# Performance work log

Measured on AMD Instinct MI355X. Metric: run time of the kernel, lower is better.

Reference implementation:

```python
import jax, jax.numpy as jnp
import numpy as np

B, S, E = 2, 2048, 1024
H, D = 16, 64
BASE = 10000.0


def rotate_half(x):
    x1, x2 = jnp.split(x, 2, axis=-1)
    return jnp.concatenate((-x2, x1), axis=-1)


def rope_cos_sin(seq_len, dim):
    inv_freq = 1.0 / (BASE ** (jnp.arange(0, dim, 2, dtype=jnp.float32) / dim))
    t = jnp.arange(seq_len, dtype=jnp.float32)
    freqs = jnp.einsum('i,j->ij', t, inv_freq)          # [S, D/2]
    emb = jnp.concatenate((freqs, freqs), axis=-1)       # [S, D]
    return jnp.cos(emb), jnp.sin(emb)


def setup_inputs() -> dict:
    key = jax.random.key(0)
    ks = jax.random.split(key, 9)
    s = 1.0 / np.sqrt(E)
    inp = {
        'x': jax.random.normal(ks[0], (B, S, E), dtype=jnp.float32),
        'mask': jnp.ones((B, S), dtype=jnp.int32),
        'Wq': jax.random.normal(ks[1], (E, H * D), dtype=jnp.float32) * s,
        'bq': jnp.zeros((H * D,), dtype=jnp.float32),
        'Wk': jax.random.normal(ks[2], (E, H * D), dtype=jnp.float32) * s,
        'bk': jnp.zeros((H * D,), dtype=jnp.float32),
        'Wv': jax.random.normal(ks[3], (E, H * D), dtype=jnp.float32) * s,
        'bv': jnp.zeros((H * D,), dtype=jnp.float32),
        'Wo': jax.random.normal(ks[4], (H * D, E), dtype=jnp.float32) * s,
        'bo': jnp.zeros((E,), dtype=jnp.float32),
    }
    return inp


def reference(x, mask, Wq, bq, Wk, bk, Wv, bv, Wo, bo):
    b, s, _ = x.shape
    scale = D ** (-0.5)
    # projections -> [B, H, S, D]
    q = (x @ Wq + bq).reshape(b, s, H, D).transpose(0, 2, 1, 3)
    k = (x @ Wk + bk).reshape(b, s, H, D).transpose(0, 2, 1, 3)
    v = (x @ Wv + bv).reshape(b, s, H, D).transpose(0, 2, 1, 3)
    # rotary position embedding
    cos, sin = rope_cos_sin(s, D)                      # [S, D]
    cos = cos[None, None]
    sin = sin[None, None]
    q = q * cos + rotate_half(q) * sin
    k = k * cos + rotate_half(k) * sin
    # scores [B, H, S, S]
    scores = jnp.einsum('bhqd,bhkd->bhqk', q, k) * scale
    # padding mask [B,1,1,S]
    scores = jnp.where(mask[:, None, None, :] == 0, -jnp.inf, scores)
    # causal mask
    i = jnp.arange(s)
    causal = jnp.where(i[None, :] > i[:, None], -jnp.inf, 0.0)  # [S, S]
    scores = scores + causal[None, None]
    attn = jax.nn.softmax(scores, axis=-1)
    ctx = jnp.einsum('bhqk,bhkd->bhqd', attn, v)
    ctx = ctx.transpose(0, 2, 1, 3).reshape(b, s, H * D)
    return ctx @ Wo + bo
```

## Files before the change

### kernel.cpp

```cpp
#include <hip/hip_runtime.h>
#include <cstdint>
#include <cstddef>

#define DEVI __device__ __forceinline__

typedef __bf16 bf16_t;
typedef __bf16 bf16x4 __attribute__((ext_vector_type(4)));
typedef __bf16 bf16x8 __attribute__((ext_vector_type(8)));
typedef float  f32x4  __attribute__((ext_vector_type(4)));
typedef float  f32x16 __attribute__((ext_vector_type(16)));
typedef unsigned short u16x4 __attribute__((ext_vector_type(4)));
typedef unsigned int   u32x4 __attribute__((ext_vector_type(4)));

static constexpr int Bz = 2, S = 2048, E = 1024, H = 16, Dh = 64;
static constexpr int M  = Bz * S;
static constexpr int N  = H * Dh;
static constexpr int Kd = E;

DEVI unsigned short f2bf(float f) {
  unsigned u = __builtin_bit_cast(unsigned, f);
  return (unsigned short)((u + 0x7fffu + ((u >> 16) & 1u)) >> 16);
}

DEVI void async_copy16(void* lds, const void* g) {
  __builtin_amdgcn_global_load_lds((__attribute__((address_space(1))) void*)(g),
                                   (__attribute__((address_space(3))) void*)(lds), 16, 0, 0);
}

DEVI void block_sync() { asm volatile("s_barrier" ::: "memory"); }
#define VMCNT4() asm volatile("s_waitcnt vmcnt(4)" ::: "memory")
#define VMCNT0() asm volatile("s_waitcnt vmcnt(0)" ::: "memory")
#define LGKM0()  asm volatile("s_waitcnt lgkmcnt(0)" ::: "memory")

DEVI unsigned cvtpk(float lo, float hi) {
  unsigned r;
  asm("v_cvt_pk_bf16_f32 %0, %1, %2" : "=v"(r) : "v"(lo), "v"(hi));
  return r;
}
DEVI void swap32(unsigned& x, unsigned& y) {
  asm("v_permlane32_swap_b32 %0, %1" : "+v"(x), "+v"(y));
}

__global__ void prep_kernel(const float* __restrict__ x, bf16_t* __restrict__ xb,
                            const float* __restrict__ Wq, const float* __restrict__ Wk,
                            const float* __restrict__ Wv, const float* __restrict__ Wo,
                            bf16_t* __restrict__ WtBase,
                            float* __restrict__ ropeC, float* __restrict__ ropeS) {
  __shared__ unsigned short tile[64][68];
  const int blk = blockIdx.x, tid = threadIdx.x;
  if (blk < 4096) {
    int i = blk * 256 + tid;
    float4 v = ((const float4*)x)[i];
    u16x4 o = { f2bf(v.x), f2bf(v.y), f2bf(v.z), f2bf(v.w) };
    ((u16x4*)xb)[i] = o;
  } else if (blk < 5120) {
    const int i = blk - 4096;
    const int z = i >> 8, rest = i & 255;
    const int n0 = (rest & 15) * 64, k0 = (rest >> 4) * 64;
    const float* W = (z == 0) ? Wq : (z == 1) ? Wk : (z == 2) ? Wv : Wo;
    unsigned short* T = (unsigned short*)(WtBase + (size_t)z * Kd * N);
    for (int e = tid; e < 1024; e += 256) {
      int r = e >> 4, c4 = (e & 15) * 4;
      float4 v = *(const float4*)(W + (size_t)(k0 + r) * N + n0 + c4);
      u16x4 o = { f2bf(v.x), f2bf(v.y), f2bf(v.z), f2bf(v.w) };
      *(u16x4*)&tile[r][c4] = o;
    }
    __syncthreads();
    for (int e = tid; e < 1024; e += 256) {
      int r = e >> 4, c4 = (e & 15) * 4;
      u16x4 o = { tile[c4][r], tile[c4 + 1][r], tile[c4 + 2][r], tile[c4 + 3][r] };
      *(u16x4*)&T[(size_t)(n0 + r) * Kd + k0 + c4] = o;
    }
  } else {
    int i = (blk - 5120) * 256 + tid;
    int pos = i >> 5, j = i & 31;
    float inv = exp2f(-(float)j * 0.41524101186092029f);
    float ang = (float)pos * inv;
    ropeC[i] = cosf(ang);
    ropeS[i] = sinf(ang);
  }
}

__global__ void vtrans_kernel(const bf16_t* __restrict__ V, bf16_t* __restrict__ Vt) {
  __shared__ unsigned short tile[64][68];
  const int bh = blockIdx.y;
  const int s0 = blockIdx.x * 64;
  const unsigned short* Vp = (const unsigned short*)V + (size_t)bh * S * Dh;
  unsigned short* Tp = (unsigned short*)Vt + (size_t)bh * S * Dh;
  const int tid = threadIdx.x;
  for (int e = tid; e < 1024; e += 256) {
    int r = e >> 4, c4 = (e & 15) * 4;
    u16x4 v = *(const u16x4*)(Vp + (size_t)(s0 + r) * Dh + c4);
    *(u16x4*)&tile[r][c4] = v;
  }
  __syncthreads();
  for (int e = tid; e < 1024; e += 256) {
    int d = e >> 4, s4 = (e & 15) * 4;
    int t = (s0 + s4) >> 5, ks = (s0 + s4) & 31;
    u16x4 o = { tile[s4][d], tile[s4 + 1][d], tile[s4 + 2][d], tile[s4 + 3][d] };
    *(u16x4*)&Tp[((size_t)t * Dh + d) * 32 + ks] = o;
  }
}


DEVI void gemm_mainloop(const bf16_t* __restrict__ A, const bf16_t* __restrict__ Bt,
                        bf16_t* sA, bf16_t* sB, int m0, int n0, f32x4 (&acc)[4][4]) {
  const int tid  = threadIdx.x;
  const int lane = tid & 63;
  const int wid  = tid >> 6;
  const int l16  = lane & 15;
  const int quad = lane >> 4;
  const int wm = (wid >> 1) * 64;
  const int wn = (wid & 1) * 64;
  const int o0 = wid * 2048 + lane * 16;
  const int o1 = o0 + 1024;
  const int r0 = o0 >> 6, c0 = o0 & 63;
  const int r1 = o1 >> 6, c1 = o1 & 63;
  const char* Ab = (const char*)A;
  const char* Bb = (const char*)Bt;
  char* sAc = (char*)sA;
  char* sBc = (char*)sB;

  for (int k0 = 0; k0 < Kd; k0 += 32) {
    __syncthreads();
    async_copy16(sAc + wid * 2048,        Ab + ((size_t)(m0 + r0) * Kd + k0) * 2 + c0);
    async_copy16(sAc + wid * 2048 + 1024, Ab + ((size_t)(m0 + r1) * Kd + k0) * 2 + c1);
    async_copy16(sBc + wid * 2048,        Bb + ((size_t)(n0 + r0) * Kd + k0) * 2 + c0);
    async_copy16(sBc + wid * 2048 + 1024, Bb + ((size_t)(n0 + r1) * Kd + k0) * 2 + c1);
    __syncthreads();
    bf16x8 af[4], bfv[4];
#pragma unroll
    for (int mi = 0; mi < 4; ++mi)
      af[mi] = *(const bf16x8*)(sA + (wm + mi * 16 + l16) * 32 + quad * 8);
#pragma unroll
    for (int ni = 0; ni < 4; ++ni)
      bfv[ni] = *(const bf16x8*)(sB + (wn + ni * 16 + l16) * 32 + quad * 8);
#pragma unroll
    for (int mi = 0; mi < 4; ++mi)
#pragma unroll
      for (int ni = 0; ni < 4; ++ni)
        acc[mi][ni] = __builtin_amdgcn_mfma_f32_16x16x32_bf16(af[mi], bfv[ni], acc[mi][ni], 0, 0, 0);
  }
}

__global__ __launch_bounds__(256, 3) void gemm_qkv_kernel(
    const bf16_t* __restrict__ xb, const bf16_t* __restrict__ WtBase,
    const float* __restrict__ bq, const float* __restrict__ bk, const float* __restrict__ bv,
    bf16_t* __restrict__ outBase,
    const float* __restrict__ ropeC, const float* __restrict__ ropeS) {
  __shared__ bf16_t sA[4096], sB[4096];
  const int z = blockIdx.z;
  const bf16_t* Bt = WtBase + (size_t)z * Kd * N;
  const float* bias = (z == 0) ? bq : (z == 1) ? bk : bv;
  unsigned short* outp = (unsigned short*)(outBase + (size_t)z * M * N);
  const int n0 = blockIdx.x * 128, m0 = blockIdx.y * 128;
  f32x4 acc[4][4] = {};
  gemm_mainloop(xb, Bt, sA, sB, m0, n0, acc);

  const int tid = threadIdx.x, lane = tid & 63, wid = tid >> 6;
  const int l16 = lane & 15, quad = lane >> 4;
  const int wm = (wid >> 1) * 64, wn = (wid & 1) * 64;
  const int cbase = n0 + wn;
  const int h = cbase >> 6;

  if (z < 2) {
    const float qs = (z == 0) ? 0.18033688011112042f : 1.0f;
#pragma unroll
    for (int mi = 0; mi < 4; ++mi)
#pragma unroll
      for (int r = 0; r < 4; ++r) {
        int t = m0 + wm + mi * 16 + quad * 4 + r;
        int bb = t >> 11, s = t & (S - 1);
        size_t obase = ((size_t)(bb * H + h) * S + s) * Dh;
#pragma unroll
        for (int np = 0; np < 2; ++np) {
          int j = np * 16 + l16;
          float cc = ropeC[s * 32 + j];
          float ss = ropeS[s * 32 + j];
          float xlo = acc[mi][np][r]     + bias[cbase + j];
          float xhi = acc[mi][np + 2][r] + bias[cbase + j + 32];
          outp[obase + j]      = f2bf((xlo * cc - xhi * ss) * qs);
          outp[obase + j + 32] = f2bf((xhi * cc + xlo * ss) * qs);
        }
      }
  } else {
#pragma unroll
    for (int mi = 0; mi < 4; ++mi)
#pragma unroll
      for (int r = 0; r < 4; ++r) {
        int t = m0 + wm + mi * 16 + quad * 4 + r;
        int bb = t >> 11, s = t & (S - 1);
        size_t obase = ((size_t)(bb * H + h) * S + s) * Dh;
#pragma unroll
        for (int ni = 0; ni < 4; ++ni) {
          int d = ni * 16 + l16;
          outp[obase + d] = f2bf(acc[mi][ni][r] + bias[cbase + d]);
        }
      }
  }
}

__global__ __launch_bounds__(256, 4) void gemm_o_kernel(
    const bf16_t* __restrict__ A, const bf16_t* __restrict__ Bt,
    const float* __restrict__ bias, float* __restrict__ out) {
  __shared__ bf16_t sA[2048], sB[4096];
  const int n0 = blockIdx.x * 128, m0 = blockIdx.y * 64;
  const int tid = threadIdx.x, lane = tid & 63, wid = tid >> 6;
  const int l16 = lane & 15, quad = lane >> 4;
  const int wm = (wid >> 1) * 32, wn = (wid & 1) * 64;
  const int rowoff = lane >> 2, col8 = (lane & 3) * 8;
  const char* Ab = (const char*)A;
  const char* Bb = (const char*)Bt;
  char* sAc = (char*)sA;
  char* sBc = (char*)sB;
  f32x4 acc[2][4] = {};

  for (int k0 = 0; k0 < Kd; k0 += 32) {
    __syncthreads();
    async_copy16(sAc + wid * 1024,
                 Ab + ((size_t)(m0 + wid * 16 + rowoff) * Kd + k0 + col8) * 2);
    async_copy16(sBc + (wid * 2) * 1024,
                 Bb + ((size_t)(n0 + wid * 32 + rowoff) * Kd + k0 + col8) * 2);
    async_copy16(sBc + (wid * 2 + 1) * 1024,
                 Bb + ((size_t)(n0 + wid * 32 + 16 + rowoff) * Kd + k0 + col8) * 2);
    __syncthreads();
    bf16x8 af[2], bfv[4];
#pragma unroll
    for (int mi = 0; mi < 2; ++mi)
      af[mi] = *(const bf16x8*)(sA + (wm + mi * 16 + l16) * 32 + quad * 8);
#pragma unroll
    for (int ni = 0; ni < 4; ++ni)
      bfv[ni] = *(const bf16x8*)(sB + (wn + ni * 16 + l16) * 32 + quad * 8);
#pragma unroll
    for (int mi = 0; mi < 2; ++mi)
#pragma unroll
      for (int ni = 0; ni < 4; ++ni)
        acc[mi][ni] = __builtin_amdgcn_mfma_f32_16x16x32_bf16(af[mi], bfv[ni], acc[mi][ni], 0, 0, 0);
  }
#pragma unroll
  for (int mi = 0; mi < 2; ++mi)
#pragma unroll
    for (int r = 0; r < 4; ++r) {
      int t = m0 + wm + mi * 16 + quad * 4 + r;
#pragma unroll
      for (int ni = 0; ni < 4; ++ni) {
        int c = n0 + wn + ni * 16 + l16;
        out[(size_t)t * N + c] = acc[mi][ni][r] + bias[c];
      }
    }
}

template <bool MASKED>
DEVI void attn32_tile(const bf16_t* __restrict__ Qp, const char* __restrict__ Kg,
                      const char* __restrict__ Vg, const int* __restrict__ mp,
                      unsigned short* __restrict__ cp, char* lds,
                      int b, int bh, int j) {
  const int tid = threadIdx.x, lane = tid & 63, wid = tid >> 6;
  const int grp = wid >> 2, w4 = wid & 3;
  const int l32 = lane & 31, hi = lane >> 5;

  const int qw = j * 128 + w4 * 32;
  const int qg = qw + l32;
  const int nIt = j + 1;
  const int gk0 = grp * nIt * 64;
  char* gB = lds + grp * 32768;

  bf16x8 qf[4];
#pragma unroll
  for (int c = 0; c < 4; ++c)
    qf[c] = *(const bf16x8*)(Qp + (size_t)(qw + l32) * Dh + c * 16 + hi * 8);
  asm volatile("" :: "v"((float)qf[3][7]));

  int sLds[4], sOff[4];
#pragma unroll
  for (int i = 0; i < 4; ++i) {
    const int s = w4 * 4 + i;
    sLds[i] = s * 1024;
    if (s < 8) {
      const int a = s >> 2, c = s & 3;
      sOff[i] = (a * 32 + l32) * 128 + c * 32 + hi * 16;
    } else {
      const int t = s - 8, a = t >> 2, v = t & 3;
      sOff[i] = a * 4096 + ((v >> 1) * 32 + l32) * 64 + (v & 1) * 32 + hi * 16;
    }
  }
  const char* gsrc = (w4 < 2) ? Kg : Vg;

  f32x16 cacc0 = {}, cacc1 = {};
  float lsum = 0.f;

  {
    const char* bp = gsrc + (size_t)gk0 * 128;
#pragma unroll
    for (int i = 0; i < 4; ++i) async_copy16(gB + sLds[i], bp + sOff[i]);
  }

  for (int kt = 0; kt < nIt; ++kt) {
    const int cur = kt & 1;
    const int kb = gk0 + kt * 64;
    unsigned long long dm = 0;
    if (kt + 1 < nIt) {
      const char* bp = gsrc + (size_t)(kb + 64) * 128;
      char* dst = gB + (cur ^ 1) * 16384;
#pragma unroll
      for (int i = 0; i < 4; ++i) async_copy16(dst + sLds[i], bp + sOff[i]);
      if (!MASKED) { VMCNT4(); }
    } else if (!MASKED) {
      VMCNT0();
    }
    if (MASKED) {
      int mk = mp[kb + lane];
      VMCNT0();
      dm = __ballot(mk == 0);
    }
    block_sync();

    const bf16_t* sT = (const bf16_t*)(gB + cur * 16384);
#pragma unroll
    for (int a = 0; a < 2; ++a) {
      f32x16 st = {};
      __builtin_amdgcn_s_setprio(1);
#pragma unroll
      for (int c = 0; c < 4; ++c) {
        bf16x8 kf = *(const bf16x8*)(sT + a * 2048 + c * 512 + lane * 8);
        st = __builtin_amdgcn_mfma_f32_32x32x16_bf16(kf, qf[c], st, 0, 0, 0);
      }
      __builtin_amdgcn_s_setprio(0);
      if (MASKED && dm) {
#pragma unroll
        for (int r = 0; r < 16; ++r)
          if ((dm >> (a * 32 + (r & 3) + 8 * (r >> 2) + 4 * hi)) & 1ull) st[r] = -1e30f;
      }
      const int kba = kb + a * 32;
      if (kba + 31 > qw) {
        const int kbase = kba + 4 * hi - qg;
#pragma unroll
        for (int r = 0; r < 16; ++r)
          if (kbase + (r & 3) + 8 * (r >> 2) > 0) st[r] = -1e30f;
      }
      unsigned P0[4], P1[4];
#pragma unroll
      for (int m = 0; m < 4; ++m) {
        float p0 = exp2f(st[4 * m + 0]), p1 = exp2f(st[4 * m + 1]);
        float p2 = exp2f(st[4 * m + 2]), p3 = exp2f(st[4 * m + 3]);
        lsum += (p0 + p1) + (p2 + p3);
        P0[m] = cvtpk(p0, p1);
        P1[m] = cvtpk(p2, p3);
      }
      swap32(P0[0], P0[1]); swap32(P1[0], P1[1]);
      swap32(P0[2], P0[3]); swap32(P1[2], P1[3]);
      u32x4 t0 = { P0[0], P1[0], P0[1], P1[1] };
      u32x4 t1 = { P0[2], P1[2], P0[3], P1[3] };
      const bf16x8 f0 = __builtin_bit_cast(bf16x8, t0);
      const bf16x8 f1 = __builtin_bit_cast(bf16x8, t1);
      __builtin_amdgcn_s_setprio(1);
      {
        bf16x8 v00 = *(const bf16x8*)(sT + 4096 + a * 2048 + 0 * 512 + lane * 8);
        cacc0 = __builtin_amdgcn_mfma_f32_32x32x16_bf16(v00, f0, cacc0, 0, 0, 0);
        bf16x8 v01 = *(const bf16x8*)(sT + 4096 + a * 2048 + 1 * 512 + lane * 8);
        cacc0 = __builtin_amdgcn_mfma_f32_32x32x16_bf16(v01, f1, cacc0, 0, 0, 0);
        bf16x8 v10 = *(const bf16x8*)(sT + 4096 + a * 2048 + 2 * 512 + lane * 8);
        cacc1 = __builtin_amdgcn_mfma_f32_32x32x16_bf16(v10, f0, cacc1, 0, 0, 0);
        bf16x8 v11 = *(const bf16x8*)(sT + 4096 + a * 2048 + 3 * 512 + lane * 8);
        cacc1 = __builtin_amdgcn_mfma_f32_32x32x16_bf16(v11, f1, cacc1, 0, 0, 0);
      }
      __builtin_amdgcn_s_setprio(0);
    }
    block_sync();
  }

  lsum += __shfl_xor(lsum, 32);
  float* reg = (float*)lds;
  if (grp == 1) {
    float* rb = reg + w4 * 2048 + l32 * 64;
#pragma unroll
    for (int m = 0; m < 4; ++m) {
      f32x4 v = { cacc0[4 * m], cacc0[4 * m + 1], cacc0[4 * m + 2], cacc0[4 * m + 3] };
      *(f32x4*)(rb + ((8 * m + 4 * hi + 4 * l32) & 63)) = v;
    }
#pragma unroll
    for (int m = 0; m < 4; ++m) {
      f32x4 v = { cacc1[4 * m], cacc1[4 * m + 1], cacc1[4 * m + 2], cacc1[4 * m + 3] };
      *(f32x4*)(rb + ((32 + 8 * m + 4 * hi + 4 * l32) & 63)) = v;
    }
    reg[8192 + w4 * 32 + l32] = lsum;
  }
  LGKM0();
  block_sync();
  if (grp == 0) {
    const float* rb = reg + w4 * 2048 + l32 * 64;
#pragma unroll
    for (int m = 0; m < 4; ++m) {
      f32x4 v = *(const f32x4*)(rb + ((8 * m + 4 * hi + 4 * l32) & 63));
      cacc0[4 * m] += v[0]; cacc0[4 * m + 1] += v[1];
      cacc0[4 * m + 2] += v[2]; cacc0[4 * m + 3] += v[3];
    }
#pragma unroll
    for (int m = 0; m < 4; ++m) {
      f32x4 v = *(const f32x4*)(rb + ((32 + 8 * m + 4 * hi + 4 * l32) & 63));
      cacc1[4 * m] += v[0]; cacc1[4 * m + 1] += v[1];
      cacc1[4 * m + 2] += v[2]; cacc1[4 * m + 3] += v[3];
    }
    const float inv = 1.0f / (lsum + reg[8192 + w4 * 32 + l32]);
    const size_t base = ((size_t)(b * S + qw + l32)) * N + (size_t)(bh & 15) * Dh;
#pragma unroll
    for (int m = 0; m < 4; ++m) {
      const int d0 = m * 8 + 4 * hi;
      u16x4 o0 = { f2bf(cacc0[4 * m + 0] * inv), f2bf(cacc0[4 * m + 1] * inv),
                   f2bf(cacc0[4 * m + 2] * inv), f2bf(cacc0[4 * m + 3] * inv) };
      *(u16x4*)&cp[base + d0] = o0;
      u16x4 o1 = { f2bf(cacc1[4 * m + 0] * inv), f2bf(cacc1[4 * m + 1] * inv),
                   f2bf(cacc1[4 * m + 2] * inv), f2bf(cacc1[4 * m + 3] * inv) };
      *(u16x4*)&cp[base + 32 + d0] = o1;
    }
  }
}

__global__ __launch_bounds__(512, 4) void attn_kernel(
    const bf16_t* __restrict__ Q, const bf16_t* __restrict__ Kb,
    const bf16_t* __restrict__ Vt, const int* __restrict__ mask,
    bf16_t* __restrict__ ctx) {
  __shared__ f32x4 ldsbuf[4096];

  const int idx = blockIdx.x;
  const int t   = idx >> 5;
  const int j   = (t < 8) ? (15 - t) : (t - 8);
  const int bh  = idx & 31;
  const int b   = bh >> 4;
  const int lane = threadIdx.x & 63;

  const bf16_t* Qp = Q + (size_t)bh * S * Dh;
  const char*   Kg = (const char*)(Kb + (size_t)bh * S * Dh);
  const char*   Vg = (const char*)(Vt + (size_t)bh * S * Dh);
  const int*    mp = mask + b * S;

  int dead = 0;
  const int4* mp4 = (const int4*)mp;
  for (int c = lane; c < S / 4; c += 64) {
    int4 m = mp4[c];
    dead |= (m.x == 0) | (m.y == 0) | (m.z == 0) | (m.w == 0);
  }
  const bool anydead = __ballot(dead != 0) != 0ull;

  unsigned short* cp = (unsigned short*)ctx;
  char* lds = (char*)ldsbuf;
  if (!anydead)
    attn32_tile<false>(Qp, Kg, Vg, mp, cp, lds, b, bh, j);
  else
    attn32_tile<true>(Qp, Kg, Vg, mp, cp, lds, b, bh, j);
}


extern "C" void kernel_launch(void* const* d_in, const int* in_sizes, int n_in,
                              void* d_out, int out_size, void* d_ws, size_t ws_size,
                              hipStream_t stream) {
  const float* x  = (const float*)d_in[0];
  const int*  msk = (const int*)d_in[1];
  const float* Wq = (const float*)d_in[2];
  const float* bq = (const float*)d_in[3];
  const float* Wk = (const float*)d_in[4];
  const float* bk = (const float*)d_in[5];
  const float* Wv = (const float*)d_in[6];
  const float* bv = (const float*)d_in[7];
  const float* Wo = (const float*)d_in[8];
  const float* bo = (const float*)d_in[9];
  float* out = (float*)d_out;
  (void)in_sizes; (void)n_in; (void)out_size; (void)ws_size;

  char* ws = (char*)d_ws;
  bf16_t* xb   = (bf16_t*)(ws);
  bf16_t* WT   = (bf16_t*)(ws + (8u  << 20));
  bf16_t* qkv  = (bf16_t*)(ws + (16u << 20));
  bf16_t* Qb   = qkv;
  bf16_t* Kbuf = qkv + (size_t)1 * M * N;
  bf16_t* Vb   = qkv + (size_t)2 * M * N;
  bf16_t* Vt   = xb;
  bf16_t* ctx  = Vb;
  float* ropeC = (float*)(ws + (40u << 20));
  float* ropeS = ropeC + (size_t)S * 32;

  prep_kernel<<<5376, 256, 0, stream>>>(x, xb, Wq, Wk, Wv, Wo, WT, ropeC, ropeS);
  gemm_qkv_kernel<<<dim3(8, 32, 3), 256, 0, stream>>>(xb, WT, bq, bk, bv, qkv, ropeC, ropeS);
  vtrans_kernel<<<dim3(32, 32), 256, 0, stream>>>(Vb, Vt);
  attn_kernel<<<512, 512, 0, stream>>>(Qb, Kbuf, Vt, msk, ctx);
  gemm_o_kernel<<<dim3(8, 64), 256, 0, stream>>>(ctx, WT + (size_t)3 * Kd * N, bo, out);
}
```

Before: 194.0 us.

## Load K/V fragments directly from global memory instead of staging through LDS

Replaces the double-buffered async global-to-LDS staging of K and V tiles, and its barriers, with per-wave direct global loads of the MFMA fragments into registers. Each iteration now processes one 32-key sub-tile, and the loop is unrolled by two so loads can overlap compute. The LDS buffer shrinks to what the final cross-group reduction needs, which may allow higher occupancy and removes block-wide syncs in the main loop. In exchange, the four waves of a group each fetch the same K/V data redundantly from cache, and latency hiding now relies on the compiler scheduling and on occupancy.

```diff
diff --git a/kernel.cpp b/kernel.cpp
--- a/kernel.cpp
+++ b/kernel.cpp
@@ -28,8 +28,6 @@
 }
 
 DEVI void block_sync() { asm volatile("s_barrier" ::: "memory"); }
-#define VMCNT4() asm volatile("s_waitcnt vmcnt(4)" ::: "memory")
-#define VMCNT0() asm volatile("s_waitcnt vmcnt(0)" ::: "memory")
 #define LGKM0()  asm volatile("s_waitcnt lgkmcnt(0)" ::: "memory")
 
 DEVI unsigned cvtpk(float lo, float hi) {
@@ -261,112 +259,79 @@
 
   const int qw = j * 128 + w4 * 32;
   const int qg = qw + l32;
-  const int nIt = j + 1;
-  const int gk0 = grp * nIt * 64;
-  char* gB = lds + grp * 32768;
+  const int nSub = 2 * (j + 1);
+  const int gk0 = grp * (j + 1) * 64;
 
   bf16x8 qf[4];
 #pragma unroll
   for (int c = 0; c < 4; ++c)
     qf[c] = *(const bf16x8*)(Qp + (size_t)(qw + l32) * Dh + c * 16 + hi * 8);
-  asm volatile("" :: "v"((float)qf[3][7]));
-
-  int sLds[4], sOff[4];
-#pragma unroll
-  for (int i = 0; i < 4; ++i) {
-    const int s = w4 * 4 + i;
-    sLds[i] = s * 1024;
-    if (s < 8) {
-      const int a = s >> 2, c = s & 3;
-      sOff[i] = (a * 32 + l32) * 128 + c * 32 + hi * 16;
-    } else {
-      const int t = s - 8, a = t >> 2, v = t & 3;
-      sOff[i] = a * 4096 + ((v >> 1) * 32 + l32) * 64 + (v & 1) * 32 + hi * 16;
-    }
-  }
-  const char* gsrc = (w4 < 2) ? Kg : Vg;
+
+  const char* kp0 = Kg + (size_t)l32 * 128 + hi * 16;
+  const char* vp0 = Vg + (size_t)l32 * 64 + hi * 16;
 
   f32x16 cacc0 = {}, cacc1 = {};
   float lsum = 0.f;
 
-  {
-    const char* bp = gsrc + (size_t)gk0 * 128;
-#pragma unroll
-    for (int i = 0; i < 4; ++i) async_copy16(gB + sLds[i], bp + sOff[i]);
-  }
-
-  for (int kt = 0; kt < nIt; ++kt) {
-    const int cur = kt & 1;
-    const int kb = gk0 + kt * 64;
+#pragma unroll 2
+  for (int kt = 0; kt < nSub; ++kt) {
+    const int kb = gk0 + kt * 32;
+    const char* kp = kp0 + (size_t)kb * 128;
+    const char* vp = vp0 + (size_t)(kb >> 5) * 4096;
+    bf16x8 kf0 = *(const bf16x8*)(kp);
+    bf16x8 kf1 = *(const bf16x8*)(kp + 32);
+    bf16x8 kf2 = *(const bf16x8*)(kp + 64);
+    bf16x8 kf3 = *(const bf16x8*)(kp + 96);
+    bf16x8 v00 = *(const bf16x8*)(vp);
+    bf16x8 v01 = *(const bf16x8*)(vp + 32);
+    bf16x8 v10 = *(const bf16x8*)(vp + 2048);
+    bf16x8 v11 = *(const bf16x8*)(vp + 2048 + 32);
     unsigned long long dm = 0;
-    if (kt + 1 < nIt) {
-      const char* bp = gsrc + (size_t)(kb + 64) * 128;
-      char* dst = gB + (cur ^ 1) * 16384;
-#pragma unroll
-      for (int i = 0; i < 4; ++i) async_copy16(dst + sLds[i], bp + sOff[i]);
-      if (!MASKED) { VMCNT4(); }
-    } else if (!MASKED) {
-      VMCNT0();
-    }
     if (MASKED) {
-      int mk = mp[kb + lane];
-      VMCNT0();
+      int mk = mp[kb + l32];
       dm = __ballot(mk == 0);
     }
-    block_sync();
-
-    const bf16_t* sT = (const bf16_t*)(gB + cur * 16384);
-#pragma unroll
-    for (int a = 0; a < 2; ++a) {
-      f32x16 st = {};
-      __builtin_amdgcn_s_setprio(1);
-#pragma unroll
-      for (int c = 0; c < 4; ++c) {
-        bf16x8 kf = *(const bf16x8*)(sT + a * 2048 + c * 512 + lane * 8);
-        st = __builtin_amdgcn_mfma_f32_32x32x16_bf16(kf, qf[c], st, 0, 0, 0);
-      }
-      __builtin_amdgcn_s_setprio(0);
-      if (MASKED && dm) {
-#pragma unroll
-        for (int r = 0; r < 16; ++r)
-          if ((dm >> (a * 32 + (r & 3) + 8 * (r >> 2) + 4 * hi)) & 1ull) st[r] = -1e30f;
-      }
-      const int kba = kb + a * 32;
-      if (kba + 31 > qw) {
-        const int kbase = kba + 4 * hi - qg;
-#pragma unroll
-        for (int r = 0; r < 16; ++r)
-          if (kbase + (r & 3) + 8 * (r >> 2) > 0) st[r] = -1e30f;
-      }
-      unsigned P0[4], P1[4];
-#pragma unroll
-      for (int m = 0; m < 4; ++m) {
-        float p0 = exp2f(st[4 * m + 0]), p1 = exp2f(st[4 * m + 1]);
-        float p2 = exp2f(st[4 * m + 2]), p3 = exp2f(st[4 * m + 3]);
-        lsum += (p0 + p1) + (p2 + p3);
-        P0[m] = cvtpk(p0, p1);
-        P1[m] = cvtpk(p2, p3);
-      }
-      swap32(P0[0], P0[1]); swap32(P1[0], P1[1]);
-      swap32(P0[2], P0[3]); swap32(P1[2], P1[3]);
-      u32x4 t0 = { P0[0], P1[0], P0[1], P1[1] };
-      u32x4 t1 = { P0[2], P1[2], P0[3], P1[3] };
-      const bf16x8 f0 = __builtin_bit_cast(bf16x8, t0);
-      const bf16x8 f1 = __builtin_bit_cast(bf16x8, t1);
-      __builtin_amdgcn_s_setprio(1);
-      {
-        bf16x8 v00 = *(const bf16x8*)(sT + 4096 + a * 2048 + 0 * 512 + lane * 8);
-        cacc0 = __builtin_amdgcn_mfma_f32_32x32x16_bf16(v00, f0, cacc0, 0, 0, 0);
-        bf16x8 v01 = *(const bf16x8*)(sT + 4096 + a * 2048 + 1 * 512 + lane * 8);
-        cacc0 = __builtin_amdgcn_mfma_f32_32x32x16_bf16(v01, f1, cacc0, 0, 0, 0);
-        bf16x8 v10 = *(const bf16x8*)(sT + 4096 + a * 2048 + 2 * 512 + lane * 8);
-        cacc1 = __builtin_amdgcn_mfma_f32_32x32x16_bf16(v10, f0, cacc1, 0, 0, 0);
-        bf16x8 v11 = *(const bf16x8*)(sT + 4096 + a * 2048 + 3 * 512 + lane * 8);
-        cacc1 = __builtin_amdgcn_mfma_f32_32x32x16_bf16(v11, f1, cacc1, 0, 0, 0);
-      }
-      __builtin_amdgcn_s_setprio(0);
-    }
-    block_sync();
+
+    f32x16 st = {};
+    __builtin_amdgcn_s_setprio(1);
+    st = __builtin_amdgcn_mfma_f32_32x32x16_bf16(kf0, qf[0], st, 0, 0, 0);
+    st = __builtin_amdgcn_mfma_f32_32x32x16_bf16(kf1, qf[1], st, 0, 0, 0);
+    st = __builtin_amdgcn_mfma_f32_32x32x16_bf16(kf2, qf[2], st, 0, 0, 0);
+    st = __builtin_amdgcn_mfma_f32_32x32x16_bf16(kf3, qf[3], st, 0, 0, 0);
+    __builtin_amdgcn_s_setprio(0);
+
+    if (MASKED && dm) {
+#pragma unroll
+      for (int r = 0; r < 16; ++r)
+        if ((dm >> ((r & 3) + 8 * (r >> 2) + 4 * hi)) & 1ull) st[r] = -1e30f;
+    }
+    if (kb + 31 > qw) {
+      const int kbase = kb + 4 * hi - qg;
+#pragma unroll
+      for (int r = 0; r < 16; ++r)
+        if (kbase + (r & 3) + 8 * (r >> 2) > 0) st[r] = -1e30f;
+    }
+    unsigned P0[4], P1[4];
+#pragma unroll
+    for (int m = 0; m < 4; ++m) {
+      float p0 = exp2f(st[4 * m + 0]), p1 = exp2f(st[4 * m + 1]);
+      float p2 = exp2f(st[4 * m + 2]), p3 = exp2f(st[4 * m + 3]);
+      lsum += (p0 + p1) + (p2 + p3);
+      P0[m] = cvtpk(p0, p1);
+      P1[m] = cvtpk(p2, p3);
+    }
+    swap32(P0[0], P0[1]); swap32(P1[0], P1[1]);
+    swap32(P0[2], P0[3]); swap32(P1[2], P1[3]);
+    u32x4 t0 = { P0[0], P1[0], P0[1], P1[1] };
+    u32x4 t1 = { P0[2], P1[2], P0[3], P1[3] };
+    const bf16x8 f0 = __builtin_bit_cast(bf16x8, t0);
+    const bf16x8 f1 = __builtin_bit_cast(bf16x8, t1);
+    __builtin_amdgcn_s_setprio(1);
+    cacc0 = __builtin_amdgcn_mfma_f32_32x32x16_bf16(v00, f0, cacc0, 0, 0, 0);
+    cacc0 = __builtin_amdgcn_mfma_f32_32x32x16_bf16(v01, f1, cacc0, 0, 0, 0);
+    cacc1 = __builtin_amdgcn_mfma_f32_32x32x16_bf16(v10, f0, cacc1, 0, 0, 0);
+    cacc1 = __builtin_amdgcn_mfma_f32_32x32x16_bf16(v11, f1, cacc1, 0, 0, 0);
+    __builtin_amdgcn_s_setprio(0);
   }
 
   lsum += __shfl_xor(lsum, 32);
@@ -420,7 +385,7 @@
     const bf16_t* __restrict__ Q, const bf16_t* __restrict__ Kb,
     const bf16_t* __restrict__ Vt, const int* __restrict__ mask,
     bf16_t* __restrict__ ctx) {
-  __shared__ f32x4 ldsbuf[4096];
+  __shared__ float ldsbuf[8448];
 
   const int idx = blockIdx.x;
   const int t   = idx >> 5;
```

Result: slower. 211.2 us (+8.9%).
